# Optimization experiments

Measured on AMD Instinct MI355X. Metric: run time of the kernel, lower is better.

## Reference

```python
import jax, jax.numpy as jnp
import numpy as np

B, D_MODEL, N, H = 2, 1024, 2048, 16
HEAD_DIM = D_MODEL // H  # 64


def _proj(x, W, b):
    # Conv1d kernel_size=1 == per-position GEMM over channels. x: [B, Cin, N]
    return jnp.einsum('oi,bin->bon', W, x) + b[:, None]


def setup_inputs() -> dict:
    key = jax.random.key(0)
    ks = jax.random.split(key, 11)
    s = 1.0 / np.sqrt(D_MODEL)
    mk = lambda k: (jax.random.uniform(k, (D_MODEL, D_MODEL), jnp.float32, -s, s))
    return {
        'query': jax.random.normal(ks[0], (B, D_MODEL, N), jnp.float32),
        'key': jax.random.normal(ks[1], (B, D_MODEL, N), jnp.float32),
        'value': jax.random.normal(ks[2], (B, D_MODEL, N), jnp.float32),
        'Wq': mk(ks[3]), 'bq': jax.random.uniform(ks[4], (D_MODEL,), jnp.float32, -s, s),
        'Wk': mk(ks[5]), 'bk': jax.random.uniform(ks[6], (D_MODEL,), jnp.float32, -s, s),
        'Wv': mk(ks[7]), 'bv': jax.random.uniform(ks[8], (D_MODEL,), jnp.float32, -s, s),
        'Wm': mk(ks[9]), 'bm': jax.random.uniform(ks[10], (D_MODEL,), jnp.float32, -s, s),
    }


def reference(query, key, value, Wq, bq, Wk, bk, Wv, bv, Wm, bm):
    b = query.shape[0]
    # project then split channels as (head_dim, heads) exactly like torch .view
    q = _proj(query, Wq, bq).reshape(b, HEAD_DIM, H, -1)  # [B, d, H, N]
    k = _proj(key, Wk, bk).reshape(b, HEAD_DIM, H, -1)
    v = _proj(value, Wv, bv).reshape(b, HEAD_DIM, H, -1)
    scores = jnp.einsum('bdhn,bdhm->bhnm', q, k) / np.sqrt(HEAD_DIM).astype(np.float32)
    prob = jax.nn.softmax(scores, axis=-1)  # [B, H, N, N]
    x = jnp.einsum('bhnm,bdhm->bdhn', prob, v)  # [B, d, H, N]
    return _proj(x.reshape(b, D_MODEL, -1), Wm, bm)  # [B, d_model, N]
```

## Files before the change

kernel.cpp:

```cpp
#include <hip/hip_runtime.h>
#include <hip/hip_bf16.h>
#include <stdint.h>

#define DM 1024
#define NS 2048
#define NH 16
#define HD 64

typedef unsigned short u16;
typedef __attribute__((ext_vector_type(8))) short short8;
typedef __attribute__((ext_vector_type(4))) short s16x4;
typedef __attribute__((ext_vector_type(8))) unsigned short u16x8;
typedef __attribute__((ext_vector_type(4))) float f32x4;
typedef __attribute__((ext_vector_type(4))) unsigned short u16x4;

#define MFMA_PV(a, b, c) __builtin_amdgcn_mfma_f32_16x16x16bf16_1k(a, b, c, 0, 0, 0)

static __device__ __forceinline__ uint32_t pkbf(float a, float b) {
  union { __hip_bfloat162 h; uint32_t u; } cv;
  cv.h = __float22bfloat162_rn(float2{a, b});
  return cv.u;
}
static __device__ __forceinline__ u16x4 pkbf4(float a, float b, float c, float d) {
  union { uint32_t u[2]; u16x4 v; } cv;
  cv.u[0] = pkbf(a, b); cv.u[1] = pkbf(c, d);
  return cv.v;
}
static __device__ __forceinline__ s16x4 pkbf4s(float a, float b, float c, float d) {
  union { uint32_t u[2]; s16x4 v; } cv;
  cv.u[0] = pkbf(a, b); cv.u[1] = pkbf(c, d);
  return cv.v;
}
static __device__ __forceinline__ void gload16(u16* lds, const u16* g) {
  auto l = (__attribute__((address_space(3))) uint32_t*)(uint32_t)(uintptr_t)lds;
  auto gp = (const __attribute__((address_space(1))) uint32_t*)(uintptr_t)g;
  __builtin_amdgcn_global_load_lds(gp, l, 16, 0, 0);
}

__global__ __launch_bounds__(256) void cvt3_k(const float* __restrict__ a,
                                              const float* __restrict__ b,
                                              const float* __restrict__ c,
                                              u16* __restrict__ oa, u16* __restrict__ ob,
                                              u16* __restrict__ oc) {
  const int y = blockIdx.y;
  const float* in = y == 0 ? a : y == 1 ? b : c;
  u16* out = y == 0 ? oa : y == 1 ? ob : oc;
  int i = (blockIdx.x * 256 + threadIdx.x) * 4;
  f32x4 v = *(const f32x4*)(in + i);
  *(u16x4*)(out + i) = pkbf4(v.x, v.y, v.z, v.w);
}

__global__ __launch_bounds__(256) void cvtp_k(const float* __restrict__ in,
                                              u16* __restrict__ out) {
  __shared__ __attribute__((aligned(16))) u16 t[4][16][68];
  const int tid = threadIdx.x;
  const int rr = tid >> 6, tl = tid & 63;
  const int row = blockIdx.x * 4 + rr;
  const float* ip = in + (size_t)row * DM;
  u16* op = out + (size_t)row * DM;
#pragma unroll
  for (int e = 0; e < 4; ++e) {
    int i = e * 256 + tl * 4;
    f32x4 v = *(const f32x4*)(ip + i);
    u16x4 bb = pkbf4(v.x, v.y, v.z, v.w);
    int d = i >> 4, h0 = i & 15;
    t[rr][h0 + 0][d] = bb.x; t[rr][h0 + 1][d] = bb.y;
    t[rr][h0 + 2][d] = bb.z; t[rr][h0 + 3][d] = bb.w;
  }
  __syncthreads();
#pragma unroll
  for (int e = 0; e < 4; ++e) {
    int j = e * 256 + tl * 4;
    int h = j >> 6, d = j & 63;
    u16x4 v;
    v.x = t[rr][h][d + 0]; v.y = t[rr][h][d + 1];
    v.z = t[rr][h][d + 2]; v.w = t[rr][h][d + 3];
    *(u16x4*)(op + j) = v;
  }
}

__global__ __launch_bounds__(256) void trf3_k(const float* __restrict__ q,
                                              const float* __restrict__ k,
                                              const float* __restrict__ v,
                                              u16* __restrict__ oq, u16* __restrict__ ok,
                                              u16* __restrict__ ov) {
  __shared__ __attribute__((aligned(16))) u16 t[64][65];
  const int z = blockIdx.z, b = z & 1, which = z >> 1;
  const float* in = which == 0 ? q : which == 1 ? k : v;
  u16* out = which == 0 ? oq : which == 1 ? ok : ov;
  const float* ip = in + (size_t)b * DM * NS;
  u16* op = out + (size_t)b * DM * NS;
  const int r0 = blockIdx.y * 64, c0 = blockIdx.x * 64;
  const int tx = threadIdx.x, ty = threadIdx.y;
#pragma unroll
  for (int j = 0; j < 4; ++j) {
    int row = ty + j * 16;
    f32x4 vv = *(const f32x4*)(ip + (size_t)(r0 + row) * NS + c0 + tx * 4);
    u16x4 bb = pkbf4(vv.x, vv.y, vv.z, vv.w);
    t[row][tx * 4 + 0] = bb.x; t[row][tx * 4 + 1] = bb.y;
    t[row][tx * 4 + 2] = bb.z; t[row][tx * 4 + 3] = bb.w;
  }
  __syncthreads();
#pragma unroll
  for (int j = 0; j < 4; ++j) {
    int crow = ty + j * 16;
    u16x4 vv;
    vv.x = t[tx * 4 + 0][crow]; vv.y = t[tx * 4 + 1][crow];
    vv.z = t[tx * 4 + 2][crow]; vv.w = t[tx * 4 + 3][crow];
    *(u16x4*)(op + (size_t)(c0 + crow) * DM + r0 + tx * 4) = vv;
  }
}

__global__ __launch_bounds__(256) void qkv_k(
    const u16* __restrict__ Xq, const u16* __restrict__ Xk, const u16* __restrict__ Xv,
    const u16* __restrict__ Wq, const u16* __restrict__ Wk, const u16* __restrict__ Wv,
    const float* __restrict__ bq, const float* __restrict__ bk, const float* __restrict__ bv,
    u16* __restrict__ QH, u16* __restrict__ KH, u16* __restrict__ VH) {
  __shared__ __attribute__((aligned(16))) u16 As[128 * 32];
  __shared__ __attribute__((aligned(16))) u16 Bs[128 * 32];
  const int z = blockIdx.z, b = z & 1, which = z >> 1;
  const u16* X = which == 0 ? Xq : which == 1 ? Xk : Xv;
  const u16* W = which == 0 ? Wq : which == 1 ? Wk : Wv;
  const float* bias = which == 0 ? bq : which == 1 ? bk : bv;
  u16* out = which == 0 ? QH : which == 1 ? KH : VH;
  const float sc = which == 0 ? 0.18033688011112042f : 1.0f;
  const int m0 = blockIdx.x * 128;
  const int c0 = blockIdx.y * 128;
  const u16* Xb = X + (size_t)b * NS * DM;
  const int tid = threadIdx.x;
  const int lane = tid & 63, w = tid >> 6;
  const int wm = w >> 1, wc = w & 1;
  const int qd = lane >> 4, ml = lane & 15;
  const int sml = (ml >> 1) & 3;

  f32x4 acc[4][4];
#pragma unroll
  for (int i = 0; i < 4; ++i)
#pragma unroll
    for (int j = 0; j < 4; ++j) acc[i][j] = (f32x4){0.f, 0.f, 0.f, 0.f};

  for (int k0 = 0; k0 < DM; k0 += 32) {
    __syncthreads();
#pragma unroll
    for (int it = 0; it < 2; ++it) {
      int ci = it * 256 + tid;
      int row = ci >> 2;
      int jg = (ci & 3) ^ ((ci >> 3) & 3);
      gload16(&As[ci * 8], Xb + (size_t)(m0 + row) * DM + k0 + jg * 8);
      gload16(&Bs[ci * 8], W + (size_t)(c0 + row) * DM + k0 + jg * 8);
    }
    __syncthreads();
    short8 af[4], bf[4];
#pragma unroll
    for (int i = 0; i < 4; ++i) {
      af[i] = *(const short8*)&As[(wm * 64 + i * 16 + ml) * 32 + ((qd ^ sml) * 8)];
      bf[i] = *(const short8*)&Bs[(wc * 64 + i * 16 + ml) * 32 + ((qd ^ sml) * 8)];
    }
#pragma unroll
    for (int mi = 0; mi < 4; ++mi)
#pragma unroll
      for (int ci2 = 0; ci2 < 4; ++ci2)
        acc[mi][ci2] = __builtin_amdgcn_mfma_f32_16x16x32_bf16(af[mi], bf[ci2],
                                                               acc[mi][ci2], 0, 0, 0);
  }

  const int cw = c0 + wc * 64;
  const int mw = m0 + wm * 64;
  float bv4[4];
#pragma unroll
  for (int ci2 = 0; ci2 < 4; ++ci2) bv4[ci2] = bias[cw + ci2 * 16 + ml];

  if (which < 2) {
    const int h = ml, d0 = cw >> 4;
    u16* ob = out + ((size_t)(b * NH + h) * NS) * HD;
#pragma unroll
    for (int mi = 0; mi < 4; ++mi) {
#pragma unroll
      for (int r = 0; r < 4; ++r) {
        int n = mw + mi * 16 + qd * 4 + r;
        *(u16x4*)(ob + (size_t)n * HD + d0) =
            pkbf4((acc[mi][0][r] + bv4[0]) * sc, (acc[mi][1][r] + bv4[1]) * sc,
                  (acc[mi][2][r] + bv4[2]) * sc, (acc[mi][3][r] + bv4[3]) * sc);
      }
    }
  } else {
#pragma unroll
    for (int ci2 = 0; ci2 < 4; ++ci2) {
      int c = cw + ci2 * 16 + ml;
      int h = c & 15, d = c >> 4;
#pragma unroll
      for (int mi = 0; mi < 4; ++mi) {
        int nb = mw + mi * 16 + qd * 4;
        *(u16x4*)(out + ((size_t)(b * NH + h) * HD + d) * NS + nb) =
            pkbf4(acc[mi][ci2][0] + bv4[ci2], acc[mi][ci2][1] + bv4[ci2],
                  acc[mi][ci2][2] + bv4[ci2], acc[mi][ci2][3] + bv4[ci2]);
      }
    }
  }
}

__global__ __launch_bounds__(256) void proj_o(const u16* __restrict__ X,
                                              const u16* __restrict__ W,
                                              const float* __restrict__ bias,
                                              float* __restrict__ out) {
  __shared__ __attribute__((aligned(16))) u16 As[64 * 32];
  __shared__ __attribute__((aligned(16))) u16 Bs[128 * 32];
  const int b = blockIdx.z;
  const int m0 = blockIdx.x * 64;
  const int c0 = blockIdx.y * 128;
  const u16* Xb = X + (size_t)b * NS * DM;
  const int tid = threadIdx.x;
  const int lane = tid & 63, w = tid >> 6;
  const int wm = w >> 1, wc = w & 1;
  const int qd = lane >> 4, ml = lane & 15;
  const int sml = (ml >> 1) & 3;

  f32x4 acc[2][4];
#pragma unroll
  for (int i = 0; i < 2; ++i)
#pragma unroll
    for (int j = 0; j < 4; ++j) acc[i][j] = (f32x4){0.f, 0.f, 0.f, 0.f};

  for (int k0 = 0; k0 < DM; k0 += 32) {
    __syncthreads();
    {
      int jg = (tid & 3) ^ ((tid >> 3) & 3);
      int row = tid >> 2;
      gload16(&As[tid * 8], Xb + (size_t)(m0 + row) * DM + k0 + jg * 8);
    }
#pragma unroll
    for (int it = 0; it < 2; ++it) {
      int ci = it * 256 + tid;
      int row = ci >> 2;
      int jg = (ci & 3) ^ ((ci >> 3) & 3);
      gload16(&Bs[ci * 8], W + (size_t)(c0 + row) * DM + k0 + jg * 8);
    }
    __syncthreads();
    short8 af[2], bf[4];
#pragma unroll
    for (int i = 0; i < 2; ++i)
      af[i] = *(const short8*)&As[(wm * 32 + i * 16 + ml) * 32 + ((qd ^ sml) * 8)];
#pragma unroll
    for (int i = 0; i < 4; ++i)
      bf[i] = *(const short8*)&Bs[(wc * 64 + i * 16 + ml) * 32 + ((qd ^ sml) * 8)];
#pragma unroll
    for (int mi = 0; mi < 2; ++mi)
#pragma unroll
      for (int ci2 = 0; ci2 < 4; ++ci2)
        acc[mi][ci2] = __builtin_amdgcn_mfma_f32_16x16x32_bf16(af[mi], bf[ci2],
                                                               acc[mi][ci2], 0, 0, 0);
  }

  const int cw = c0 + wc * 64;
  const int mw = m0 + wm * 32;
#pragma unroll
  for (int ci2 = 0; ci2 < 4; ++ci2) {
    int c = cw + ci2 * 16 + ml;
    float bv = bias[c];
#pragma unroll
    for (int mi = 0; mi < 2; ++mi) {
      int nb = mw + mi * 16 + qd * 4;
      f32x4 v;
      v.x = acc[mi][ci2][0] + bv; v.y = acc[mi][ci2][1] + bv;
      v.z = acc[mi][ci2][2] + bv; v.w = acc[mi][ci2][3] + bv;
      *(f32x4*)(out + ((size_t)b * DM + c) * NS + nb) = v;
    }
  }
}

__global__ __launch_bounds__(256) void attn_k(const u16* __restrict__ Q,
                                              const u16* __restrict__ K,
                                              const u16* __restrict__ V,
                                              u16* __restrict__ XO) {
  __shared__ __attribute__((aligned(16))) u16 Ks[2 * 2 * 2048];
  __shared__ __attribute__((aligned(16))) u16 Vs[2 * 2 * 2048];
  const int bh = blockIdx.y, b = bh >> 4, h = bh & 15;
  const int n0 = blockIdx.x * 64;
  const u16* Qb = Q + (size_t)bh * NS * HD;
  const u16* Kb = K + (size_t)bh * NS * HD;
  const u16* Vb = V + (size_t)bh * HD * NS;
  const int tid = threadIdx.x, lane = tid & 63, w = tid >> 6;
  const int qd = lane >> 4, ml = lane & 15;
  const int sml = (ml >> 1) & 3;

  short8 aq[2];
  {
    const u16* qr = Qb + (size_t)(n0 + w * 16 + ml) * HD + qd * 8;
    aq[0] = *(const short8*)qr;
    aq[1] = *(const short8*)(qr + 32);
  }

  const int srow = tid >> 2;
  const int jg = (tid & 3) ^ ((tid >> 3) & 3);

#pragma unroll
  for (int s = 0; s < 2; ++s) {
    gload16(&Ks[s * 2048 + tid * 8], Kb + (size_t)srow * HD + s * 32 + jg * 8);
    gload16(&Vs[s * 2048 + tid * 8], Vb + (size_t)srow * NS + s * 32 + jg * 8);
  }
  __syncthreads();

  f32x4 O[4];
#pragma unroll
  for (int i = 0; i < 4; ++i) O[i] = (f32x4){0.f, 0.f, 0.f, 0.f};
  f32x4 lsum4 = (f32x4){0.f, 0.f, 0.f, 0.f};

  for (int kb = 0; kb < NS / 64; ++kb) {
    const int cur = kb & 1, nxt = cur ^ 1;
    if (kb < NS / 64 - 1) {
#pragma unroll
      for (int s = 0; s < 2; ++s) {
        gload16(&Ks[(nxt * 2 + s) * 2048 + tid * 8],
                Kb + (size_t)((kb + 1) * 64 + srow) * HD + s * 32 + jg * 8);
        gload16(&Vs[(nxt * 2 + s) * 2048 + tid * 8],
                Vb + (size_t)srow * NS + (kb + 1) * 64 + s * 32 + jg * 8);
      }
    }

    const u16* kbase = &Ks[cur * 2 * 2048];
    f32x4 S[4];
#pragma unroll
    for (int f = 0; f < 4; ++f) S[f] = (f32x4){0.f, 0.f, 0.f, 0.f};
#pragma unroll
    for (int f = 0; f < 4; ++f)
#pragma unroll
      for (int ks = 0; ks < 2; ++ks) {
        short8 bk = *(const short8*)&kbase[ks * 2048 + (f * 16 + ml) * 32 +
                                           ((qd ^ sml) * 8)];
        S[f] = __builtin_amdgcn_mfma_f32_16x16x32_bf16(bk, aq[ks], S[f], 0, 0, 0);
      }

    s16x4 pf[4];
#pragma unroll
    for (int f = 0; f < 4; ++f) {
      f32x4 p;
      p.x = __builtin_amdgcn_exp2f(S[f][0]);
      p.y = __builtin_amdgcn_exp2f(S[f][1]);
      p.z = __builtin_amdgcn_exp2f(S[f][2]);
      p.w = __builtin_amdgcn_exp2f(S[f][3]);
      lsum4 += p;
      pf[f] = pkbf4s(p.x, p.y, p.z, p.w);
    }

    const u16* vbase = &Vs[cur * 2 * 2048];
#pragma unroll
    for (int t = 0; t < 4; ++t) {
      const int vs = t >> 1;
      const int voff = ((((t & 1) * 2 + (qd >> 1)) ^ sml) * 8) + (qd & 1) * 4;
#pragma unroll
      for (int df = 0; df < 4; ++df) {
        s16x4 vb = *(const s16x4*)&vbase[vs * 2048 + (df * 16 + ml) * 32 + voff];
        O[df] = MFMA_PV(vb, pf[t], O[df]);
      }
    }
    __syncthreads();
  }

  float lsum = (lsum4.x + lsum4.y) + (lsum4.z + lsum4.w);
  lsum += __shfl_xor(lsum, 16);
  lsum += __shfl_xor(lsum, 32);
  const float linv = 1.f / lsum;

  u16* xb = XO + ((size_t)(b * NS) + n0 + w * 16 + ml) * DM + h * 64;
#pragma unroll
  for (int df = 0; df < 4; ++df) {
    *(u16x4*)(xb + df * 16 + qd * 4) =
        pkbf4(O[df][0] * linv, O[df][1] * linv, O[df][2] * linv, O[df][3] * linv);
  }
}

extern "C" void kernel_launch(void* const* d_in, const int* in_sizes, int n_in,
                              void* d_out, int out_size, void* d_ws, size_t ws_size,
                              hipStream_t stream) {
  const float* query = (const float*)d_in[0];
  const float* key = (const float*)d_in[1];
  const float* value = (const float*)d_in[2];
  const float* Wq = (const float*)d_in[3]; const float* bq = (const float*)d_in[4];
  const float* Wk = (const float*)d_in[5]; const float* bk = (const float*)d_in[6];
  const float* Wv = (const float*)d_in[7]; const float* bv = (const float*)d_in[8];
  const float* Wm = (const float*)d_in[9]; const float* bm = (const float*)d_in[10];

  u16* ws = (u16*)d_ws;
  const size_t TS = (size_t)2 * NS * DM;
  const size_t WSZ = (size_t)DM * DM;
  u16* XTq = ws;
  u16* XTk = ws + TS;
  u16* XTv = ws + 2 * TS;
  u16* QH = ws + 3 * TS;
  u16* KH = ws + 4 * TS;
  u16* VH = ws + 5 * TS;
  u16* Wqb = ws + 6 * TS;
  u16* Wkb = Wqb + WSZ;
  u16* Wvb = Wkb + WSZ;
  u16* Wmb = Wvb + WSZ;
  u16* XO = XTq;

  cvt3_k<<<dim3(WSZ / 1024, 3), 256, 0, stream>>>(Wq, Wk, Wv, Wqb, Wkb, Wvb);
  cvtp_k<<<DM / 4, 256, 0, stream>>>(Wm, Wmb);

  dim3 tb(16, 16);
  trf3_k<<<dim3(NS / 64, DM / 64, 6), tb, 0, stream>>>(query, key, value, XTq, XTk, XTv);

  qkv_k<<<dim3(NS / 128, DM / 128, 6), 256, 0, stream>>>(
      XTq, XTk, XTv, Wqb, Wkb, Wvb, bq, bk, bv, QH, KH, VH);

  attn_k<<<dim3(NS / 64, 32), 256, 0, stream>>>(QH, KH, VH, XO);

  proj_o<<<dim3(NS / 64, DM / 128, 2), 256, 0, stream>>>(XO, Wmb, bm, (float*)d_out);
}
```

Baseline: 237.3 us.

## Split attention key range in two halves and combine partials in a separate kernel

The attention kernel now splits the key/value sequence into two halves across blockIdx.z. This doubles the block count and halves the serial loop length per block. Each half writes unnormalized fp32 outputs and row sums to workspace, and a new combine kernel adds them, normalizes and packs to bf16. The cost is large extra fp32 global traffic, one more launch, and more workspace. The combination is only correct because both halves share the same (unshifted) exponent reference.

```diff
diff --git a/kernel.cpp b/kernel.cpp
--- a/kernel.cpp
+++ b/kernel.cpp
@@ -271,14 +271,17 @@
 __global__ __launch_bounds__(256) void attn_k(const u16* __restrict__ Q,
                                               const u16* __restrict__ K,
                                               const u16* __restrict__ V,
-                                              u16* __restrict__ XO) {
+                                              float* __restrict__ O0,
+                                              float* __restrict__ O1,
+                                              float* __restrict__ lp) {
   __shared__ __attribute__((aligned(16))) u16 Ks[2 * 2 * 2048];
   __shared__ __attribute__((aligned(16))) u16 Vs[2 * 2 * 2048];
   const int bh = blockIdx.y, b = bh >> 4, h = bh & 15;
+  const int half = blockIdx.z;
   const int n0 = blockIdx.x * 64;
   const u16* Qb = Q + (size_t)bh * NS * HD;
-  const u16* Kb = K + (size_t)bh * NS * HD;
-  const u16* Vb = V + (size_t)bh * HD * NS;
+  const u16* Kb = K + (size_t)bh * NS * HD + (size_t)half * (NS / 2) * HD;
+  const u16* Vb = V + (size_t)bh * HD * NS + (size_t)half * (NS / 2);
   const int tid = threadIdx.x, lane = tid & 63, w = tid >> 6;
   const int qd = lane >> 4, ml = lane & 15;
   const int sml = (ml >> 1) & 3;
@@ -305,9 +308,10 @@
   for (int i = 0; i < 4; ++i) O[i] = (f32x4){0.f, 0.f, 0.f, 0.f};
   f32x4 lsum4 = (f32x4){0.f, 0.f, 0.f, 0.f};
 
-  for (int kb = 0; kb < NS / 64; ++kb) {
+  const int NT = (NS / 2) / 64;
+  for (int kb = 0; kb < NT; ++kb) {
     const int cur = kb & 1, nxt = cur ^ 1;
-    if (kb < NS / 64 - 1) {
+    if (kb < NT - 1) {
 #pragma unroll
       for (int s = 0; s < 2; ++s) {
         gload16(&Ks[(nxt * 2 + s) * 2048 + tid * 8],
@@ -359,14 +363,32 @@
   float lsum = (lsum4.x + lsum4.y) + (lsum4.z + lsum4.w);
   lsum += __shfl_xor(lsum, 16);
   lsum += __shfl_xor(lsum, 32);
-  const float linv = 1.f / lsum;
-
-  u16* xb = XO + ((size_t)(b * NS) + n0 + w * 16 + ml) * DM + h * 64;
-#pragma unroll
-  for (int df = 0; df < 4; ++df) {
-    *(u16x4*)(xb + df * 16 + qd * 4) =
-        pkbf4(O[df][0] * linv, O[df][1] * linv, O[df][2] * linv, O[df][3] * linv);
-  }
+  if (lane < 16)
+    lp[((size_t)(half * 32 + bh)) * NS + n0 + w * 16 + ml] = lsum;
+
+  float* Op = half ? O1 : O0;
+  float* xb = Op + ((size_t)(b * NS) + n0 + w * 16 + ml) * DM + h * 64;
+#pragma unroll
+  for (int df = 0; df < 4; ++df)
+    *(f32x4*)(xb + df * 16 + qd * 4) = O[df];
+}
+
+__global__ __launch_bounds__(256) void comb_k(const float* __restrict__ O0,
+                                              const float* __restrict__ O1,
+                                              const float* __restrict__ lp,
+                                              u16* __restrict__ XO) {
+  const size_t t = (size_t)blockIdx.x * 256 + threadIdx.x;
+  const int j4 = (int)(t & (DM / 4 - 1));
+  const int n = (int)((t >> 8) & (NS - 1));
+  const int b = (int)(t >> 19);
+  const int h = j4 >> 4;
+  f32x4 o0 = *(const f32x4*)(O0 + t * 4);
+  f32x4 o1 = *(const f32x4*)(O1 + t * 4);
+  const float l0 = lp[((size_t)(b * 16 + h)) * NS + n];
+  const float l1 = lp[((size_t)(32 + b * 16 + h)) * NS + n];
+  const float linv = 1.f / (l0 + l1);
+  *(u16x4*)(XO + t * 4) = pkbf4((o0.x + o1.x) * linv, (o0.y + o1.y) * linv,
+                                (o0.z + o1.z) * linv, (o0.w + o1.w) * linv);
 }
 
 extern "C" void kernel_launch(void* const* d_in, const int* in_sizes, int n_in,
@@ -393,7 +415,10 @@
   u16* Wkb = Wqb + WSZ;
   u16* Wvb = Wkb + WSZ;
   u16* Wmb = Wvb + WSZ;
-  u16* XO = XTq;
+  float* O0 = (float*)ws;
+  float* O1 = (float*)(ws + 6 * TS + 4 * WSZ);
+  float* lp = O1 + (size_t)2 * NS * DM;
+  u16* XO = XTv;
 
   cvt3_k<<<dim3(WSZ / 1024, 3), 256, 0, stream>>>(Wq, Wk, Wv, Wqb, Wkb, Wvb);
   cvtp_k<<<DM / 4, 256, 0, stream>>>(Wm, Wmb);
@@ -404,7 +429,8 @@
   qkv_k<<<dim3(NS / 128, DM / 128, 6), 256, 0, stream>>>(
       XTq, XTk, XTv, Wqb, Wkb, Wvb, bq, bk, bv, QH, KH, VH);
 
-  attn_k<<<dim3(NS / 64, 32), 256, 0, stream>>>(QH, KH, VH, XO);
+  attn_k<<<dim3(NS / 64, 32, 2), 256, 0, stream>>>(QH, KH, VH, O0, O1, lp);
+  comb_k<<<(2 * NS * DM / 4) / 256, 256, 0, stream>>>(O0, O1, lp, XO);
 
   proj_o<<<dim3(NS / 64, DM / 128, 2), 256, 0, stream>>>(XO, Wmb, bm, (float*)d_out);
 }
```

Result: slower. 244.5 us (+3.1%).

## Double attention query tile per block and merge weight conversion kernels

Applied to the files above, without the earlier changes.

The attention kernel now handles 128 query rows per block, two 16-row sub-tiles per wave, so every K and V fragment read from LDS feeds two MFMAs and the K/V global traffic per query halves. The grid shrinks to 512 blocks and per-thread register use roughly doubles for accumulators and probabilities. Separately, the two weight-conversion kernels (plain and transposing) are merged into one launch to cut launch overhead. The merged kernel calls __syncthreads only in the y==3 branch, which is uniform per block, so it stays safe.

```diff
diff --git a/kernel.cpp b/kernel.cpp
--- a/kernel.cpp
+++ b/kernel.cpp
@@ -37,45 +37,36 @@
   __builtin_amdgcn_global_load_lds(gp, l, 16, 0, 0);
 }
 
-__global__ __launch_bounds__(256) void cvt3_k(const float* __restrict__ a,
-                                              const float* __restrict__ b,
-                                              const float* __restrict__ c,
-                                              u16* __restrict__ oa, u16* __restrict__ ob,
-                                              u16* __restrict__ oc) {
-  const int y = blockIdx.y;
-  const float* in = y == 0 ? a : y == 1 ? b : c;
-  u16* out = y == 0 ? oa : y == 1 ? ob : oc;
-  int i = (blockIdx.x * 256 + threadIdx.x) * 4;
-  f32x4 v = *(const f32x4*)(in + i);
-  *(u16x4*)(out + i) = pkbf4(v.x, v.y, v.z, v.w);
-}
-
-__global__ __launch_bounds__(256) void cvtp_k(const float* __restrict__ in,
-                                              u16* __restrict__ out) {
-  __shared__ __attribute__((aligned(16))) u16 t[4][16][68];
-  const int tid = threadIdx.x;
-  const int rr = tid >> 6, tl = tid & 63;
-  const int row = blockIdx.x * 4 + rr;
-  const float* ip = in + (size_t)row * DM;
-  u16* op = out + (size_t)row * DM;
-#pragma unroll
-  for (int e = 0; e < 4; ++e) {
-    int i = e * 256 + tl * 4;
+__global__ __launch_bounds__(256) void cvtw_k(
+    const float* __restrict__ wq, const float* __restrict__ wk,
+    const float* __restrict__ wv, const float* __restrict__ wm,
+    u16* __restrict__ oq, u16* __restrict__ ok,
+    u16* __restrict__ ov, u16* __restrict__ om) {
+  __shared__ __attribute__((aligned(16))) u16 t[16][68];
+  const int y = blockIdx.y, tid = threadIdx.x;
+  if (y < 3) {
+    const float* in = y == 0 ? wq : y == 1 ? wk : wv;
+    u16* out = y == 0 ? oq : y == 1 ? ok : ov;
+    int i = (blockIdx.x * 256 + tid) * 4;
+    f32x4 v = *(const f32x4*)(in + i);
+    *(u16x4*)(out + i) = pkbf4(v.x, v.y, v.z, v.w);
+  } else {
+    const int row = blockIdx.x;
+    const float* ip = wm + (size_t)row * DM;
+    u16* op = om + (size_t)row * DM;
+    int i = tid * 4;
     f32x4 v = *(const f32x4*)(ip + i);
     u16x4 bb = pkbf4(v.x, v.y, v.z, v.w);
     int d = i >> 4, h0 = i & 15;
-    t[rr][h0 + 0][d] = bb.x; t[rr][h0 + 1][d] = bb.y;
-    t[rr][h0 + 2][d] = bb.z; t[rr][h0 + 3][d] = bb.w;
-  }
-  __syncthreads();
-#pragma unroll
-  for (int e = 0; e < 4; ++e) {
-    int j = e * 256 + tl * 4;
-    int h = j >> 6, d = j & 63;
-    u16x4 v;
-    v.x = t[rr][h][d + 0]; v.y = t[rr][h][d + 1];
-    v.z = t[rr][h][d + 2]; v.w = t[rr][h][d + 3];
-    *(u16x4*)(op + j) = v;
+    t[h0 + 0][d] = bb.x; t[h0 + 1][d] = bb.y;
+    t[h0 + 2][d] = bb.z; t[h0 + 3][d] = bb.w;
+    __syncthreads();
+    int j = tid * 4;
+    int h = j >> 6, dd = j & 63;
+    u16x4 o;
+    o.x = t[h][dd + 0]; o.y = t[h][dd + 1];
+    o.z = t[h][dd + 2]; o.w = t[h][dd + 3];
+    *(u16x4*)(op + j) = o;
   }
 }
 
@@ -275,7 +266,7 @@
   __shared__ __attribute__((aligned(16))) u16 Ks[2 * 2 * 2048];
   __shared__ __attribute__((aligned(16))) u16 Vs[2 * 2 * 2048];
   const int bh = blockIdx.y, b = bh >> 4, h = bh & 15;
-  const int n0 = blockIdx.x * 64;
+  const int n0 = blockIdx.x * 128;
   const u16* Qb = Q + (size_t)bh * NS * HD;
   const u16* Kb = K + (size_t)bh * NS * HD;
   const u16* Vb = V + (size_t)bh * HD * NS;
@@ -283,11 +274,12 @@
   const int qd = lane >> 4, ml = lane & 15;
   const int sml = (ml >> 1) & 3;
 
-  short8 aq[2];
-  {
-    const u16* qr = Qb + (size_t)(n0 + w * 16 + ml) * HD + qd * 8;
-    aq[0] = *(const short8*)qr;
-    aq[1] = *(const short8*)(qr + 32);
+  short8 aq[2][2];
+#pragma unroll
+  for (int s = 0; s < 2; ++s) {
+    const u16* qr = Qb + (size_t)(n0 + w * 32 + s * 16 + ml) * HD + qd * 8;
+    aq[s][0] = *(const short8*)qr;
+    aq[s][1] = *(const short8*)(qr + 32);
   }
 
   const int srow = tid >> 2;
@@ -300,10 +292,13 @@
   }
   __syncthreads();
 
-  f32x4 O[4];
-#pragma unroll
-  for (int i = 0; i < 4; ++i) O[i] = (f32x4){0.f, 0.f, 0.f, 0.f};
-  f32x4 lsum4 = (f32x4){0.f, 0.f, 0.f, 0.f};
+  f32x4 O[2][4];
+#pragma unroll
+  for (int s = 0; s < 2; ++s)
+#pragma unroll
+    for (int i = 0; i < 4; ++i) O[s][i] = (f32x4){0.f, 0.f, 0.f, 0.f};
+  f32x4 ls0 = (f32x4){0.f, 0.f, 0.f, 0.f};
+  f32x4 ls1 = (f32x4){0.f, 0.f, 0.f, 0.f};
 
   for (int kb = 0; kb < NS / 64; ++kb) {
     const int cur = kb & 1, nxt = cur ^ 1;
@@ -318,28 +313,27 @@
     }
 
     const u16* kbase = &Ks[cur * 2 * 2048];
-    f32x4 S[4];
-#pragma unroll
-    for (int f = 0; f < 4; ++f) S[f] = (f32x4){0.f, 0.f, 0.f, 0.f};
-#pragma unroll
-    for (int f = 0; f < 4; ++f)
+    s16x4 pf[2][4];
+#pragma unroll
+    for (int f = 0; f < 4; ++f) {
+      f32x4 S0 = (f32x4){0.f, 0.f, 0.f, 0.f};
+      f32x4 S1 = (f32x4){0.f, 0.f, 0.f, 0.f};
 #pragma unroll
       for (int ks = 0; ks < 2; ++ks) {
         short8 bk = *(const short8*)&kbase[ks * 2048 + (f * 16 + ml) * 32 +
                                            ((qd ^ sml) * 8)];
-        S[f] = __builtin_amdgcn_mfma_f32_16x16x32_bf16(bk, aq[ks], S[f], 0, 0, 0);
+        S0 = __builtin_amdgcn_mfma_f32_16x16x32_bf16(bk, aq[0][ks], S0, 0, 0, 0);
+        S1 = __builtin_amdgcn_mfma_f32_16x16x32_bf16(bk, aq[1][ks], S1, 0, 0, 0);
       }
-
-    s16x4 pf[4];
-#pragma unroll
-    for (int f = 0; f < 4; ++f) {
       f32x4 p;
-      p.x = __builtin_amdgcn_exp2f(S[f][0]);
-      p.y = __builtin_amdgcn_exp2f(S[f][1]);
-      p.z = __builtin_amdgcn_exp2f(S[f][2]);
-      p.w = __builtin_amdgcn_exp2f(S[f][3]);
-      lsum4 += p;
-      pf[f] = pkbf4s(p.x, p.y, p.z, p.w);
+      p.x = __builtin_amdgcn_exp2f(S0[0]); p.y = __builtin_amdgcn_exp2f(S0[1]);
+      p.z = __builtin_amdgcn_exp2f(S0[2]); p.w = __builtin_amdgcn_exp2f(S0[3]);
+      ls0 += p;
+      pf[0][f] = pkbf4s(p.x, p.y, p.z, p.w);
+      p.x = __builtin_amdgcn_exp2f(S1[0]); p.y = __builtin_amdgcn_exp2f(S1[1]);
+      p.z = __builtin_amdgcn_exp2f(S1[2]); p.w = __builtin_amdgcn_exp2f(S1[3]);
+      ls1 += p;
+      pf[1][f] = pkbf4s(p.x, p.y, p.z, p.w);
     }
 
     const u16* vbase = &Vs[cur * 2 * 2048];
@@ -350,22 +344,27 @@
 #pragma unroll
       for (int df = 0; df < 4; ++df) {
         s16x4 vb = *(const s16x4*)&vbase[vs * 2048 + (df * 16 + ml) * 32 + voff];
-        O[df] = MFMA_PV(vb, pf[t], O[df]);
+        O[0][df] = MFMA_PV(vb, pf[0][t], O[0][df]);
+        O[1][df] = MFMA_PV(vb, pf[1][t], O[1][df]);
       }
     }
     __syncthreads();
   }
 
-  float lsum = (lsum4.x + lsum4.y) + (lsum4.z + lsum4.w);
-  lsum += __shfl_xor(lsum, 16);
-  lsum += __shfl_xor(lsum, 32);
-  const float linv = 1.f / lsum;
-
-  u16* xb = XO + ((size_t)(b * NS) + n0 + w * 16 + ml) * DM + h * 64;
-#pragma unroll
-  for (int df = 0; df < 4; ++df) {
-    *(u16x4*)(xb + df * 16 + qd * 4) =
-        pkbf4(O[df][0] * linv, O[df][1] * linv, O[df][2] * linv, O[df][3] * linv);
+#pragma unroll
+  for (int s = 0; s < 2; ++s) {
+    f32x4 l4 = s == 0 ? ls0 : ls1;
+    float lsum = (l4.x + l4.y) + (l4.z + l4.w);
+    lsum += __shfl_xor(lsum, 16);
+    lsum += __shfl_xor(lsum, 32);
+    const float linv = 1.f / lsum;
+    u16* xb = XO + ((size_t)(b * NS) + n0 + w * 32 + s * 16 + ml) * DM + h * 64;
+#pragma unroll
+    for (int df = 0; df < 4; ++df) {
+      *(u16x4*)(xb + df * 16 + qd * 4) =
+          pkbf4(O[s][df][0] * linv, O[s][df][1] * linv,
+                O[s][df][2] * linv, O[s][df][3] * linv);
+    }
   }
 }
 
@@ -395,8 +394,7 @@
   u16* Wmb = Wvb + WSZ;
   u16* XO = XTq;
 
-  cvt3_k<<<dim3(WSZ / 1024, 3), 256, 0, stream>>>(Wq, Wk, Wv, Wqb, Wkb, Wvb);
-  cvtp_k<<<DM / 4, 256, 0, stream>>>(Wm, Wmb);
+  cvtw_k<<<dim3(WSZ / 1024, 4), 256, 0, stream>>>(Wq, Wk, Wv, Wm, Wqb, Wkb, Wvb, Wmb);
 
   dim3 tb(16, 16);
   trf3_k<<<dim3(NS / 64, DM / 64, 6), tb, 0, stream>>>(query, key, value, XTq, XTk, XTv);
@@ -404,7 +402,7 @@
   qkv_k<<<dim3(NS / 128, DM / 128, 6), 256, 0, stream>>>(
       XTq, XTk, XTv, Wqb, Wkb, Wvb, bq, bk, bv, QH, KH, VH);
 
-  attn_k<<<dim3(NS / 64, 32), 256, 0, stream>>>(QH, KH, VH, XO);
+  attn_k<<<dim3(NS / 128, 32), 256, 0, stream>>>(QH, KH, VH, XO);
 
   proj_o<<<dim3(NS / 64, DM / 128, 2), 256, 0, stream>>>(XO, Wmb, bm, (float*)d_out);
 }
```

Measured after the change: 236.9 us. Within noise of the previous version (-0.1%).
